# Kernel tuning notes

Hardware: AMD Instinct MI355X
Metric: run time of the kernel (lower is better)

## Reference

```python
import jax, jax.numpy as jnp
import numpy as np

# config (matches init_kwargs)
B, H, N, D = 2, 8, 2048, 64
ALPHA = 1.0        # < 2 -> power-law kernel branch
D_INT = 4.0        # d_intrinsic
BW = 1.0           # bandwidth
A = 0.5            # dual-sided degree-normalization exponent
R = 1.0            # sphere_radius
MASK_VAL = 10000.0
EPS = 1e-7


def setup_inputs() -> dict:
    key = jax.random.key(0)
    k1, k2, k3, k4 = jax.random.split(key, 4)
    Q = jax.random.normal(k1, (B, H, N, D), dtype=jnp.float32)
    K = jax.random.normal(k2, (B, H, N, D), dtype=jnp.float32)
    V = jax.random.normal(k3, (B, H, N, D), dtype=jnp.float32)
    mask = jax.random.randint(k4, (B, N), 0, 2).astype(jnp.int32)
    return {"Q": Q, "K": K, "V": V, "mask": mask}


def reference(Q, K, V, mask) -> jnp.ndarray:
    # geodesic distance on the sphere: acos(clamp(QK^T)) * radius  [B,H,N,N]
    qk = jnp.einsum('bhnd,bhmd->bhnm', Q, K)
    g_dist = jnp.arccos(jnp.clip(qk, -1.0 + EPS, 1.0 - EPS)) * R
    # key-side padding mask: [B,N] -> [B,1,1,N]
    g_dist = jnp.where(mask[:, None, None, :] == 0, MASK_VAL, g_dist)
    # power-law kernel (alpha < 2 branch)
    attn_score = (1.0 + g_dist / jnp.sqrt(BW)) ** (-D_INT - ALPHA)
    # dual-sided degree normalization (a != 0 branch)
    n_r = jnp.sum(attn_score, axis=-1)   # row degrees [B,H,N]
    n_c = jnp.sum(attn_score, axis=-2)   # col degrees [B,H,N]
    k_tilde = (n_r ** (-A))[..., :, None] * attn_score * (n_c ** (-A))[..., None, :]
    # F.normalize(p=1, dim=3)
    attn = k_tilde / jnp.maximum(jnp.sum(jnp.abs(k_tilde), axis=-1, keepdims=True), 1e-12)
    # dropout p=0.0 -> identity
    return jnp.einsum('bhnm,bhmd->bhnd', attn, V)
```

## Files before the change

kernel.cpp:

```cpp
#include <hip/hip_runtime.h>
#include <hip/hip_bf16.h>
#include <math.h>

#define B_ 2
#define H_ 8
#define N_ 2048
#define D_ 64
#define BH_ 16
#define NT_ (N_/64)
#define LS 72
#define LSW (LS/2)

typedef __attribute__((ext_vector_type(8))) short short8;
typedef __attribute__((ext_vector_type(4))) float float4v;

__device__ __forceinline__ unsigned packbf2(float a, float b){
  __hip_bfloat162 h = __float22bfloat162_rn(make_float2(a, b));
  return *(unsigned*)&h;
}
__device__ __forceinline__ void split2(float a, float b, unsigned& hi, unsigned& lo){
  hi = packbf2(a, b);
  float ha = __uint_as_float(hi << 16);
  float hb = __uint_as_float(hi & 0xFFFF0000u);
  lo = packbf2(a - ha, b - hb);
}
__device__ __forceinline__ void load_split8(const float* p, short8& hi8, short8& lo8){
  float4v v0 = *(const float4v*)p;
  float4v v1 = *(const float4v*)(p + 4);
  unsigned h0,h1,h2,h3,l0,l1,l2,l3;
  split2(v0.x, v0.y, h0, l0);
  split2(v0.z, v0.w, h1, l1);
  split2(v1.x, v1.y, h2, l2);
  split2(v1.z, v1.w, h3, l3);
  unsigned ph[4] = {h0,h1,h2,h3};
  unsigned pl[4] = {l0,l1,l2,l3};
  hi8 = *(short8*)ph;
  lo8 = *(short8*)pl;
}

__device__ __forceinline__ float score_fn(float qk, float masked){
  float ax = fminf(fabsf(qk), 1.0f - 1e-7f);
  float t  = __builtin_amdgcn_sqrtf(1.0f - ax);
  float p  = __builtin_fmaf(__builtin_fmaf(__builtin_fmaf(-0.0187293f, ax, 0.0742610f),
                                           ax, -0.2121144f), ax, 1.5707288f);
  float t2 = t * p;
  float g  = (qk >= 0.0f) ? t2 : (3.14159265358979f - t2);
  g = (masked != 0.0f) ? 10000.0f : g;
  float w1 = 1.0f + g;
  float w2 = w1*w1;
  float w4 = w2*w2;
  float w5 = w4*w1;
  return __builtin_amdgcn_rcpf(w5);
}

template<bool STORE>
__global__ __launch_bounds__(256) void k1_score(
    const float* __restrict__ Q, const float* __restrict__ K,
    const int* __restrict__ mask, float* __restrict__ ncw,
    unsigned short* __restrict__ S)
{
  __shared__ float msk[64];
  __shared__ float red[64*4];

  const int kt = blockIdx.x, bh = blockIdx.y, rz = blockIdx.z;
  const int nz = gridDim.z;
  const int tid = threadIdx.x;
  const int wv = tid>>6, lane = tid&63, quad = lane>>4, l15 = lane&15;

  const float* Qg = Q + (size_t)bh*N_*D_;
  const float* Kg = K + (size_t)bh*N_*D_;

  short8 khi[4][2], klo[4][2];
  #pragma unroll
  for (int s=0;s<4;++s){
    const float* kp = Kg + (size_t)(kt*64 + s*16 + l15)*D_ + quad*8;
    load_split8(kp,      khi[s][0], klo[s][0]);
    load_split8(kp + 32, khi[s][1], klo[s][1]);
  }
  if (tid < 64)
    msk[tid] = (mask[(bh>>3)*N_ + kt*64 + tid] == 0) ? 1.f : 0.f;
  __syncthreads();

  float cs[4][4];
  #pragma unroll
  for (int s=0;s<4;++s)
    #pragma unroll
    for (int i=0;i<4;++i) cs[s][i] = 0.f;

  const int iters = NT_/nz;
  for (int rti=0; rti<iters; ++rti){
    const int rt = rz*iters + rti;
    const float* qp = Qg + (size_t)(rt*64 + wv*16 + l15)*D_ + quad*8;
    short8 bhi[2], blo[2];
    load_split8(qp,      bhi[0], blo[0]);
    load_split8(qp + 32, bhi[1], blo[1]);

    const size_t nrow = (size_t)(bh*NT_ + kt)*N_ + (size_t)rt*64 + wv*16 + l15;
    #pragma unroll
    for (int s=0;s<4;++s){
      float4v c = {0.f,0.f,0.f,0.f};
      #pragma unroll
      for (int cc=0; cc<2; ++cc){
        c = __builtin_amdgcn_mfma_f32_16x16x32_bf16(khi[s][cc], bhi[cc], c, 0,0,0);
        c = __builtin_amdgcn_mfma_f32_16x16x32_bf16(khi[s][cc], blo[cc], c, 0,0,0);
        c = __builtin_amdgcn_mfma_f32_16x16x32_bf16(klo[s][cc], bhi[cc], c, 0,0,0);
      }
      int kl = s*16 + quad*4;
      float sc0 = score_fn(c[0], msk[kl+0]);
      float sc1 = score_fn(c[1], msk[kl+1]);
      float sc2 = score_fn(c[2], msk[kl+2]);
      float sc3 = score_fn(c[3], msk[kl+3]);
      cs[s][0]+=sc0; cs[s][1]+=sc1; cs[s][2]+=sc2; cs[s][3]+=sc3;
      if (STORE){
        uint2 pk;
        pk.x = packbf2(sc0, sc1);
        pk.y = packbf2(sc2, sc3);
        *(uint2*)&S[nrow*64 + kl] = pk;
      }
    }
  }

  #pragma unroll
  for (int s=0;s<4;++s)
    #pragma unroll
    for (int i=0;i<4;++i){
      float v2 = cs[s][i];
      v2 += __shfl_xor(v2, 1);
      v2 += __shfl_xor(v2, 2);
      v2 += __shfl_xor(v2, 4);
      v2 += __shfl_xor(v2, 8);
      cs[s][i] = v2;
    }
  if (l15 == 0){
    #pragma unroll
    for (int s=0;s<4;++s)
      #pragma unroll
      for (int i=0;i<4;++i)
        red[(s*16 + quad*4 + i)*4 + wv] = cs[s][i];
  }
  __syncthreads();
  if (tid < 64){
    float t = red[tid*4+0] + red[tid*4+1] + red[tid*4+2] + red[tid*4+3];
    if (STORE) atomicAdd(&ncw[bh*N_ + kt*64 + tid], t);
    else       ncw[bh*N_ + kt*64 + tid] = 1.0f / sqrtf(t);
  }
}

__global__ __launch_bounds__(256) void k2_pack(
    const float* __restrict__ V, const float* __restrict__ nc,
    unsigned short* __restrict__ Vw)
{
  __shared__ float T[64*65];
  __shared__ float wrow[64];
  const int mt = blockIdx.x, bh = blockIdx.y;
  const int tid = threadIdx.x;
  const float* Vg = V + (size_t)bh*N_*D_;
  const float* ncg = nc + (size_t)bh*N_;
  unsigned short* Fb = Vw + ((size_t)(bh*NT_ + mt)*10)*512;

  {
    int m = tid >> 2;
    int d0 = (tid & 3) * 16;
    int gm = mt*64 + m;
    float wm = 1.0f / sqrtf(fmaxf(ncg[gm], 1e-30f));
    if (d0 == 0) wrow[m] = wm;
    #pragma unroll
    for (int j=0;j<4;++j){
      float4v v = *(const float4v*)(Vg + (size_t)gm*D_ + d0 + j*4);
      T[(d0+j*4+0)*65 + m] = v.x*wm;
      T[(d0+j*4+1)*65 + m] = v.y*wm;
      T[(d0+j*4+2)*65 + m] = v.z*wm;
      T[(d0+j*4+3)*65 + m] = v.w*wm;
    }
  }
  __syncthreads();

  for (int idx = tid; idx < 640; idx += 256){
    int f = idx >> 6, lane = idx & 63;
    int quad = lane >> 4, l15 = lane & 15;
    int s2 = f >> 1, cc = f & 1;
    int m0 = cc*32 + quad*8;
    unsigned pk[4];
    if (s2 < 4){
      int d = s2*16 + l15;
      #pragma unroll
      for (int j=0;j<4;++j)
        pk[j] = packbf2(T[d*65 + m0 + 2*j], T[d*65 + m0 + 2*j + 1]);
    } else if (l15 == 0){
      #pragma unroll
      for (int j=0;j<4;++j)
        pk[j] = packbf2(wrow[m0 + 2*j], wrow[m0 + 2*j + 1]);
    } else {
      pk[0]=pk[1]=pk[2]=pk[3]=0u;
    }
    *(short8*)(Fb + ((size_t)f*64 + lane)*8) = *(short8*)pk;
  }
}

__global__ __launch_bounds__(1024) void k3_lds(
    const unsigned short* __restrict__ S, const unsigned short* __restrict__ Vw,
    float* __restrict__ out)
{
  __shared__ unsigned short Vs[2*2*10*512];

  const int rtp = blockIdx.x, bh = blockIdx.y;
  const int tid = threadIdx.x;
  const int wvid = tid >> 6;
  const int g    = wvid >> 3;
  const int slot = wvid & 7;
  const int lane = tid & 63, quad = lane >> 4, l15 = lane & 15;

  const int row = rtp*128 + slot*16 + l15;

  float4v acc[4];
  #pragma unroll
  for (int i=0;i<4;++i) acc[i] = (float4v){0.f,0.f,0.f,0.f};
  float4v c5 = {0.f,0.f,0.f,0.f};

  for (int c = tid; c < 1280; c += 1024){
    const int gg = (c >= 640) ? 1 : 0;
    const int rem = c - gg*640;
    const int f = rem >> 6, ln = rem & 63;
    const int kt = gg*16;
    *(short8*)&Vs[(((0*2 + gg)*10 + f) << 9) + ln*8] =
      *(const short8*)&Vw[(((size_t)(bh*NT_ + kt)*10 + f) << 9) + ln*8];
  }
  short8 npf0, npf1;
  {
    const size_t sb = ((size_t)(bh*NT_ + g*16)*N_ + row)*64;
    npf0 = *(const short8*)&S[sb + quad*8];
    npf1 = *(const short8*)&S[sb + 32 + quad*8];
  }
  __syncthreads();

  for (int it = 0; it < 16; ++it){
    const int cur = it & 1, nxt = cur ^ 1;
    short8 pf0 = npf0, pf1 = npf1;
    if (it < 15){
      const size_t sb = ((size_t)(bh*NT_ + g*16 + it + 1)*N_ + row)*64;
      npf0 = *(const short8*)&S[sb + quad*8];
      npf1 = *(const short8*)&S[sb + 32 + quad*8];
      for (int c = tid; c < 1280; c += 1024){
        const int gg = (c >= 640) ? 1 : 0;
        const int rem = c - gg*640;
        const int f = rem >> 6, ln = rem & 63;
        const int kt2 = gg*16 + it + 1;
        *(short8*)&Vs[(((nxt*2 + gg)*10 + f) << 9) + ln*8] =
          *(const short8*)&Vw[(((size_t)(bh*NT_ + kt2)*10 + f) << 9) + ln*8];
      }
    }
    const unsigned short* Fl = &Vs[((cur*2 + g)*10) << 9] + (size_t)lane*8;
    short8 va[10];
    #pragma unroll
    for (int f=0; f<10; ++f)
      va[f] = *(const short8*)(Fl + ((size_t)f << 9));

    #pragma unroll
    for (int s2=0;s2<4;++s2){
      acc[s2] = __builtin_amdgcn_mfma_f32_16x16x32_bf16(va[s2*2+0], pf0, acc[s2], 0,0,0);
      acc[s2] = __builtin_amdgcn_mfma_f32_16x16x32_bf16(va[s2*2+1], pf1, acc[s2], 0,0,0);
    }
    c5 = __builtin_amdgcn_mfma_f32_16x16x32_bf16(va[8], pf0, c5, 0,0,0);
    c5 = __builtin_amdgcn_mfma_f32_16x16x32_bf16(va[9], pf1, c5, 0,0,0);

    __syncthreads();
  }

  float* Red = (float*)Vs;
  if (g == 1){
    float* Rr = Red + (size_t)(slot*16 + l15)*68;
    #pragma unroll
    for (int s2=0;s2<4;++s2)
      #pragma unroll
      for (int i=0;i<4;++i)
        Rr[s2*16 + quad*4 + i] = acc[s2][i];
    if (quad == 0) Rr[64] = c5[0];
  }
  __syncthreads();
  if (g == 0){
    const float* Rr = Red + (size_t)(slot*16 + l15)*68;
    #pragma unroll
    for (int s2=0;s2<4;++s2)
      #pragma unroll
      for (int i=0;i<4;++i)
        acc[s2][i] += Rr[s2*16 + quad*4 + i];
    float rs = __shfl(c5[0], l15) + Rr[64];
    float inv = 1.0f / fmaxf(rs, 1e-12f);

    float* Og = out + (size_t)bh*N_*D_ + (size_t)row*D_;
    #pragma unroll
    for (int s2=0;s2<4;++s2)
      #pragma unroll
      for (int i=0;i<4;++i)
        Og[s2*16 + quad*4 + i] = acc[s2][i] * inv;
  }
}

__global__ __launch_bounds__(256) void spop_pass2(
    const float* __restrict__ Q, const float* __restrict__ K,
    const float* __restrict__ V, const int* __restrict__ mask,
    const float* __restrict__ w, float* __restrict__ out)
{
  __shared__ unsigned short Khi[64*LS], Klo[64*LS];
  __shared__ unsigned short Vt[64*LS];
  __shared__ unsigned short Ps[64*LS];
  __shared__ float msk[64], wms[64];

  const int rt = blockIdx.x, bh = blockIdx.y, b = bh>>3;
  const int tid = threadIdx.x;
  const int wv = tid>>6, lane = tid&63, quad = lane>>4, l15 = lane&15;

  const float* Qg = Q + (size_t)bh*N_*D_;
  const float* Kg = K + (size_t)bh*N_*D_;
  const float* Vg = V + (size_t)bh*N_*D_;

  short8 qhi[2], qlo[2];
  {
    const float* qp = Qg + (size_t)(rt*64 + wv*16 + l15)*D_ + quad*8;
    load_split8(qp,      qhi[0], qlo[0]);
    load_split8(qp + 32, qhi[1], qlo[1]);
  }

  float4v acc[4];
  #pragma unroll
  for (int i=0;i<4;++i) acc[i] = (float4v){0.f,0.f,0.f,0.f};
  float rs = 0.f;

  for (int kt=0; kt<NT_; ++kt){
    __syncthreads();
    #pragma unroll
    for (int it=0; it<4; ++it){
      int idx = tid + it*256;
      int r = idx>>4, d4 = (idx&15)<<2;
      const float4v v = *(const float4v*)(Kg + (size_t)(kt*64 + r)*D_ + d4);
      unsigned h0,l0,h1,l1;
      split2(v.x, v.y, h0, l0);
      split2(v.z, v.w, h1, l1);
      unsigned* KhiW = (unsigned*)Khi; unsigned* KloW = (unsigned*)Klo;
      int base = r*LSW + (d4>>1);
      KhiW[base] = h0; KhiW[base+1] = h1;
      KloW[base] = l0; KloW[base+1] = l1;
    }
    #pragma unroll
    for (int it=0; it<2; ++it){
      int u = tid + it*256;
      int kp = u & 31;
      int d4 = (u>>5)<<2;
      const float* vp = Vg + (size_t)(kt*64 + kp*2)*D_ + d4;
      float4v a0 = *(const float4v*)vp;
      float4v a1 = *(const float4v*)(vp + D_);
      unsigned* VtW = (unsigned*)Vt;
      VtW[(d4+0)*LSW + kp] = packbf2(a0.x, a1.x);
      VtW[(d4+1)*LSW + kp] = packbf2(a0.y, a1.y);
      VtW[(d4+2)*LSW + kp] = packbf2(a0.z, a1.z);
      VtW[(d4+3)*LSW + kp] = packbf2(a0.w, a1.w);
    }
    if (tid < 64){
      int gk = kt*64 + tid;
      msk[tid] = (mask[b*N_ + gk] == 0) ? 1.f : 0.f;
      wms[tid] = w[bh*N_ + gk];
    }
    __syncthreads();

    #pragma unroll
    for (int s=0;s<4;++s){
      float4v c = {0.f,0.f,0.f,0.f};
      #pragma unroll
      for (int cc=0; cc<2; ++cc){
        const short8 ahi = *(const short8*)&Khi[(s*16+l15)*LS + cc*32 + quad*8];
        const short8 alo = *(const short8*)&Klo[(s*16+l15)*LS + cc*32 + quad*8];
        c = __builtin_amdgcn_mfma_f32_16x16x32_bf16(ahi, qhi[cc], c, 0,0,0);
        c = __builtin_amdgcn_mfma_f32_16x16x32_bf16(ahi, qlo[cc], c, 0,0,0);
        c = __builtin_amdgcn_mfma_f32_16x16x32_bf16(alo, qhi[cc], c, 0,0,0);
      }
      int kl = s*16 + quad*4;
      float sc0 = score_fn(c[0], msk[kl+0]) * wms[kl+0];
      float sc1 = score_fn(c[1], msk[kl+1]) * wms[kl+1];
      float sc2 = score_fn(c[2], msk[kl+2]) * wms[kl+2];
      float sc3 = score_fn(c[3], msk[kl+3]) * wms[kl+3];
      rs += (sc0 + sc1) + (sc2 + sc3);
      unsigned* PsW = (unsigned*)Ps;
      int pb = (wv*16 + l15)*LSW + (kl>>1);
      PsW[pb]   = packbf2(sc0, sc1);
      PsW[pb+1] = packbf2(sc2, sc3);
    }

    short8 pf[2];
    pf[0] = *(const short8*)&Ps[(wv*16+l15)*LS +  0 + quad*8];
    pf[1] = *(const short8*)&Ps[(wv*16+l15)*LS + 32 + quad*8];
    #pragma unroll
    for (int s2=0;s2<4;++s2){
      #pragma unroll
      for (int cc=0; cc<2; ++cc){
        const short8 av = *(const short8*)&Vt[(s2*16+l15)*LS + cc*32 + quad*8];
        acc[s2] = __builtin_amdgcn_mfma_f32_16x16x32_bf16(av, pf[cc], acc[s2], 0,0,0);
      }
    }
  }

  rs += __shfl_xor(rs, 16);
  rs += __shfl_xor(rs, 32);
  float inv = 1.0f / fmaxf(rs, 1e-12f);

  float* Og = out + (size_t)bh*N_*D_ + (size_t)(rt*64 + wv*16 + l15)*D_;
  #pragma unroll
  for (int s2=0;s2<4;++s2)
    #pragma unroll
    for (int i=0;i<4;++i)
      Og[s2*16 + quad*4 + i] = acc[s2][i] * inv;
}

extern "C" void kernel_launch(void* const* d_in, const int* in_sizes, int n_in,
                              void* d_out, int out_size, void* d_ws, size_t ws_size,
                              hipStream_t stream) {
  (void)in_sizes; (void)n_in; (void)out_size;
  const float* Q   = (const float*)d_in[0];
  const float* K   = (const float*)d_in[1];
  const float* V   = (const float*)d_in[2];
  const int*  mask = (const int*)d_in[3];
  float* out = (float*)d_out;

  const size_t nc_bytes = (size_t)BH_*N_*sizeof(float);
  const size_t vw_off   = 131072;
  const size_t vw_bytes = (size_t)BH_*NT_*10*512*2;
  const size_t s_off    = vw_off + vw_bytes;
  const size_t S_bytes  = (size_t)2*BH_*N_*N_;
  const size_t need     = s_off + S_bytes;

  if (ws_size >= need){
    float* nc = (float*)d_ws;
    unsigned short* Vw = (unsigned short*)((char*)d_ws + vw_off);
    unsigned short* S  = (unsigned short*)((char*)d_ws + s_off);
    hipMemsetAsync(nc, 0, nc_bytes, stream);
    k1_score<true><<<dim3(NT_, BH_, 4), 256, 0, stream>>>(Q, K, mask, nc, S);
    k2_pack<<<dim3(NT_, BH_), 256, 0, stream>>>(V, nc, Vw);
    k3_lds<<<dim3(N_/128, BH_), 1024, 0, stream>>>(S, Vw, out);
  } else {
    float* w = (float*)d_ws;
    k1_score<false><<<dim3(NT_, BH_, 1), 256, 0, stream>>>(Q, K, mask, w, nullptr);
    spop_pass2<<<dim3(NT_, BH_), 256, 0, stream>>>(Q, K, V, mask, w, out);
  }
}
```

Before: 184.9 us.

## Pre-split Q/K to bf16 hi/lo, drop score masking, tile S in MFMA layout

Adds a pre-pass that splits Q and K into bf16 hi/lo arrays once, so the score kernel loads ready-made operands instead of re-splitting fp32 Q for every key tile. The key mask leaves the score loop: masked columns are zeroed through the column weight in the V-pack kernel, so column degrees of masked keys are no longer exact but their contribution vanishes. S is stored in a blocked fragment layout so the PV kernel reads contiguous 16-byte chunks, and the next Q fragment is software-prefetched. The cost is extra workspace and an additional kernel launch.

After: 173.9 us. 1.06x faster.

```diff
diff --git a/kernel.cpp b/kernel.cpp
--- a/kernel.cpp
+++ b/kernel.cpp
@@ -38,7 +38,19 @@
   lo8 = *(short8*)pl;
 }
 
-__device__ __forceinline__ float score_fn(float qk, float masked){
+__device__ __forceinline__ float score_fn(float qk){
+  float ax = fminf(fabsf(qk), 1.0f - 1e-7f);
+  float t  = __builtin_amdgcn_sqrtf(1.0f - ax);
+  float p  = __builtin_fmaf(__builtin_fmaf(__builtin_fmaf(-0.0187293f, ax, 0.0742610f),
+                                           ax, -0.2121144f), ax, 1.5707288f);
+  float t2 = t * p;
+  float g  = (qk >= 0.0f) ? t2 : (3.14159265358979f - t2);
+  float w1 = 1.0f + g;
+  float w2 = w1*w1;
+  float w4 = w2*w2;
+  return __builtin_amdgcn_rcpf(w4*w1);
+}
+__device__ __forceinline__ float score_fn_m(float qk, float masked){
   float ax = fminf(fabsf(qk), 1.0f - 1e-7f);
   float t  = __builtin_amdgcn_sqrtf(1.0f - ax);
   float p  = __builtin_fmaf(__builtin_fmaf(__builtin_fmaf(-0.0187293f, ax, 0.0742610f),
@@ -49,37 +61,56 @@
   float w1 = 1.0f + g;
   float w2 = w1*w1;
   float w4 = w2*w2;
-  float w5 = w4*w1;
-  return __builtin_amdgcn_rcpf(w5);
-}
-
-template<bool STORE>
+  return __builtin_amdgcn_rcpf(w4*w1);
+}
+
+__global__ __launch_bounds__(256) void k0_split(
+    const float* __restrict__ Q, const float* __restrict__ K,
+    unsigned short* __restrict__ Qh, unsigned short* __restrict__ Ql,
+    unsigned short* __restrict__ Kh, unsigned short* __restrict__ Kl)
+{
+  size_t i = (size_t)blockIdx.x*256 + threadIdx.x;
+  const size_t tot = (size_t)BH_*N_*D_/8;
+  const float* src; unsigned short *dh, *dl;
+  if (i < tot){ src = Q; dh = Qh; dl = Ql; }
+  else        { src = K; dh = Kh; dl = Kl; i -= tot; }
+  short8 hi, lo;
+  load_split8(src + i*8, hi, lo);
+  *(short8*)&dh[i*8] = hi;
+  *(short8*)&dl[i*8] = lo;
+}
+
+template<bool PRE>
 __global__ __launch_bounds__(256) void k1_score(
-    const float* __restrict__ Q, const float* __restrict__ K,
-    const int* __restrict__ mask, float* __restrict__ ncw,
-    unsigned short* __restrict__ S)
+    const float* __restrict__ Qf, const float* __restrict__ Kf,
+    const unsigned short* __restrict__ Qh, const unsigned short* __restrict__ Ql,
+    const unsigned short* __restrict__ Kh, const unsigned short* __restrict__ Kl,
+    float* __restrict__ ncw, unsigned short* __restrict__ S)
 {
-  __shared__ float msk[64];
   __shared__ float red[64*4];
-
   const int kt = blockIdx.x, bh = blockIdx.y, rz = blockIdx.z;
   const int nz = gridDim.z;
   const int tid = threadIdx.x;
   const int wv = tid>>6, lane = tid&63, quad = lane>>4, l15 = lane&15;
 
-  const float* Qg = Q + (size_t)bh*N_*D_;
-  const float* Kg = K + (size_t)bh*N_*D_;
-
   short8 khi[4][2], klo[4][2];
-  #pragma unroll
-  for (int s=0;s<4;++s){
-    const float* kp = Kg + (size_t)(kt*64 + s*16 + l15)*D_ + quad*8;
-    load_split8(kp,      khi[s][0], klo[s][0]);
-    load_split8(kp + 32, khi[s][1], klo[s][1]);
-  }
-  if (tid < 64)
-    msk[tid] = (mask[(bh>>3)*N_ + kt*64 + tid] == 0) ? 1.f : 0.f;
-  __syncthreads();
+  if constexpr (PRE){
+    #pragma unroll
+    for (int s=0;s<4;++s){
+      const size_t r = (size_t)(bh*N_ + kt*64 + s*16 + l15)*D_ + quad*8;
+      khi[s][0] = *(const short8*)&Kh[r];
+      khi[s][1] = *(const short8*)&Kh[r+32];
+      klo[s][0] = *(const short8*)&Kl[r];
+      klo[s][1] = *(const short8*)&Kl[r+32];
+    }
+  } else {
+    #pragma unroll
+    for (int s=0;s<4;++s){
+      const float* kp = Kf + (size_t)(bh*N_ + kt*64 + s*16 + l15)*D_ + quad*8;
+      load_split8(kp,      khi[s][0], klo[s][0]);
+      load_split8(kp + 32, khi[s][1], klo[s][1]);
+    }
+  }
 
   float cs[4][4];
   #pragma unroll
@@ -88,36 +119,59 @@
     for (int i=0;i<4;++i) cs[s][i] = 0.f;
 
   const int iters = NT_/nz;
+  const int rt0 = rz*iters;
+
+  const size_t qoff0 = (size_t)(bh*N_ + rt0*64 + wv*16 + l15)*D_ + quad*8;
+  const unsigned lconst = (unsigned)(((quad>>1)<<7) + (l15<<3) + ((quad&1)<<2));
+  unsigned short* Sp = S + ((((size_t)(bh*NT_ + kt)*NT_ + rt0)*4 + wv)<<10) + lconst;
+
+  short8 qh0,qh1,ql0,ql1;
+  if constexpr (PRE){
+    const unsigned short* qp = Qh + qoff0;
+    const unsigned short* lp = Ql + qoff0;
+    qh0 = *(const short8*)qp;      qh1 = *(const short8*)(qp+32);
+    ql0 = *(const short8*)lp;      ql1 = *(const short8*)(lp+32);
+  } else {
+    const float* qp = Qf + qoff0;
+    load_split8(qp,      qh0, ql0);
+    load_split8(qp + 32, qh1, ql1);
+  }
+
   for (int rti=0; rti<iters; ++rti){
-    const int rt = rz*iters + rti;
-    const float* qp = Qg + (size_t)(rt*64 + wv*16 + l15)*D_ + quad*8;
-    short8 bhi[2], blo[2];
-    load_split8(qp,      bhi[0], blo[0]);
-    load_split8(qp + 32, bhi[1], blo[1]);
-
-    const size_t nrow = (size_t)(bh*NT_ + kt)*N_ + (size_t)rt*64 + wv*16 + l15;
+    short8 nh0,nh1,nl0,nl1;
+    const size_t qoffn = qoff0 + (size_t)(rti + ((rti+1<iters) ? 1 : 0))*4096;
+    if constexpr (PRE){
+      const unsigned short* qp = Qh + qoffn;
+      const unsigned short* lp = Ql + qoffn;
+      nh0 = *(const short8*)qp;    nh1 = *(const short8*)(qp+32);
+      nl0 = *(const short8*)lp;    nl1 = *(const short8*)(lp+32);
+    } else {
+      const float* qp = Qf + qoffn;
+      load_split8(qp,      nh0, nl0);
+      load_split8(qp + 32, nh1, nl1);
+    }
+
     #pragma unroll
     for (int s=0;s<4;++s){
       float4v c = {0.f,0.f,0.f,0.f};
-      #pragma unroll
-      for (int cc=0; cc<2; ++cc){
-        c = __builtin_amdgcn_mfma_f32_16x16x32_bf16(khi[s][cc], bhi[cc], c, 0,0,0);
-        c = __builtin_amdgcn_mfma_f32_16x16x32_bf16(khi[s][cc], blo[cc], c, 0,0,0);
-        c = __builtin_amdgcn_mfma_f32_16x16x32_bf16(klo[s][cc], bhi[cc], c, 0,0,0);
-      }
-      int kl = s*16 + quad*4;
-      float sc0 = score_fn(c[0], msk[kl+0]);
-      float sc1 = score_fn(c[1], msk[kl+1]);
-      float sc2 = score_fn(c[2], msk[kl+2]);
-      float sc3 = score_fn(c[3], msk[kl+3]);
+      c = __builtin_amdgcn_mfma_f32_16x16x32_bf16(khi[s][0], qh0, c, 0,0,0);
+      c = __builtin_amdgcn_mfma_f32_16x16x32_bf16(khi[s][0], ql0, c, 0,0,0);
+      c = __builtin_amdgcn_mfma_f32_16x16x32_bf16(klo[s][0], qh0, c, 0,0,0);
+      c = __builtin_amdgcn_mfma_f32_16x16x32_bf16(khi[s][1], qh1, c, 0,0,0);
+      c = __builtin_amdgcn_mfma_f32_16x16x32_bf16(khi[s][1], ql1, c, 0,0,0);
+      c = __builtin_amdgcn_mfma_f32_16x16x32_bf16(klo[s][1], qh1, c, 0,0,0);
+      float sc0 = score_fn(c[0]);
+      float sc1 = score_fn(c[1]);
+      float sc2 = score_fn(c[2]);
+      float sc3 = score_fn(c[3]);
       cs[s][0]+=sc0; cs[s][1]+=sc1; cs[s][2]+=sc2; cs[s][3]+=sc3;
-      if (STORE){
-        uint2 pk;
-        pk.x = packbf2(sc0, sc1);
-        pk.y = packbf2(sc2, sc3);
-        *(uint2*)&S[nrow*64 + kl] = pk;
-      }
-    }
+      uint2 pk;
+      pk.x = packbf2(sc0, sc1);
+      pk.y = packbf2(sc2, sc3);
+      *(uint2*)(Sp + (s<<8)) = pk;
+    }
+    Sp += 4096;
+    qh0=nh0; qh1=nh1; ql0=nl0; ql1=nl1;
   }
 
   #pragma unroll
@@ -141,14 +195,13 @@
   __syncthreads();
   if (tid < 64){
     float t = red[tid*4+0] + red[tid*4+1] + red[tid*4+2] + red[tid*4+3];
-    if (STORE) atomicAdd(&ncw[bh*N_ + kt*64 + tid], t);
-    else       ncw[bh*N_ + kt*64 + tid] = 1.0f / sqrtf(t);
+    atomicAdd(&ncw[bh*N_ + kt*64 + tid], t);
   }
 }
 
 __global__ __launch_bounds__(256) void k2_pack(
     const float* __restrict__ V, const float* __restrict__ nc,
-    unsigned short* __restrict__ Vw)
+    const int* __restrict__ mask, unsigned short* __restrict__ Vw)
 {
   __shared__ float T[64*65];
   __shared__ float wrow[64];
@@ -162,7 +215,8 @@
     int m = tid >> 2;
     int d0 = (tid & 3) * 16;
     int gm = mt*64 + m;
-    float wm = 1.0f / sqrtf(fmaxf(ncg[gm], 1e-30f));
+    float wm = (mask[(bh>>3)*N_ + gm] == 0) ? 0.0f
+             : (1.0f / sqrtf(fmaxf(ncg[gm], 1e-30f)));
     if (d0 == 0) wrow[m] = wm;
     #pragma unroll
     for (int j=0;j<4;++j){
@@ -211,6 +265,10 @@
   const int lane = tid & 63, quad = lane >> 4, l15 = lane & 15;
 
   const int row = rtp*128 + slot*16 + l15;
+  const int rt  = rtp*2 + (slot>>2);
+
+  const size_t sb0 = ((((size_t)bh*NT_ + g*16)*NT_ + rt)*4 + (size_t)(slot&3))*1024
+                   + (size_t)quad*128 + (size_t)l15*8;
 
   float4v acc[4];
   #pragma unroll
@@ -226,20 +284,17 @@
       *(const short8*)&Vw[(((size_t)(bh*NT_ + kt)*10 + f) << 9) + ln*8];
   }
   short8 npf0, npf1;
-  {
-    const size_t sb = ((size_t)(bh*NT_ + g*16)*N_ + row)*64;
-    npf0 = *(const short8*)&S[sb + quad*8];
-    npf1 = *(const short8*)&S[sb + 32 + quad*8];
-  }
+  npf0 = *(const short8*)&S[sb0];
+  npf1 = *(const short8*)&S[sb0 + 512];
   __syncthreads();
 
   for (int it = 0; it < 16; ++it){
     const int cur = it & 1, nxt = cur ^ 1;
     short8 pf0 = npf0, pf1 = npf1;
     if (it < 15){
-      const size_t sb = ((size_t)(bh*NT_ + g*16 + it + 1)*N_ + row)*64;
-      npf0 = *(const short8*)&S[sb + quad*8];
-      npf1 = *(const short8*)&S[sb + 32 + quad*8];
+      const size_t sb = sb0 + (size_t)(it+1)*131072;
+      npf0 = *(const short8*)&S[sb];
+      npf1 = *(const short8*)&S[sb + 512];
       for (int c = tid; c < 1280; c += 1024){
         const int gg = (c >= 640) ? 1 : 0;
         const int rem = c - gg*640;
@@ -293,6 +348,84 @@
       #pragma unroll
       for (int i=0;i<4;++i)
         Og[s2*16 + quad*4 + i] = acc[s2][i] * inv;
+  }
+}
+
+__global__ __launch_bounds__(256) void k1_fallback(
+    const float* __restrict__ Q, const float* __restrict__ K,
+    const int* __restrict__ mask, float* __restrict__ ncw)
+{
+  __shared__ float msk[64];
+  __shared__ float red[64*4];
+  const int kt = blockIdx.x, bh = blockIdx.y;
+  const int tid = threadIdx.x;
+  const int wv = tid>>6, lane = tid&63, quad = lane>>4, l15 = lane&15;
+
+  const float* Qg = Q + (size_t)bh*N_*D_;
+  const float* Kg = K + (size_t)bh*N_*D_;
+
+  short8 khi[4][2], klo[4][2];
+  #pragma unroll
+  for (int s=0;s<4;++s){
+    const float* kp = Kg + (size_t)(kt*64 + s*16 + l15)*D_ + quad*8;
+    load_split8(kp,      khi[s][0], klo[s][0]);
+    load_split8(kp + 32, khi[s][1], klo[s][1]);
+  }
+  if (tid < 64)
+    msk[tid] = (mask[(bh>>3)*N_ + kt*64 + tid] == 0) ? 1.f : 0.f;
+  __syncthreads();
+
+  float cs[4][4];
+  #pragma unroll
+  for (int s=0;s<4;++s)
+    #pragma unroll
+    for (int i=0;i<4;++i) cs[s][i] = 0.f;
+
+  for (int rt=0; rt<NT_; ++rt){
+    const float* qp = Qg + (size_t)(rt*64 + wv*16 + l15)*D_ + quad*8;
+    short8 bhi[2], blo[2];
+    load_split8(qp,      bhi[0], blo[0]);
+    load_split8(qp + 32, bhi[1], blo[1]);
+
+    #pragma unroll
+    for (int s=0;s<4;++s){
+      float4v c = {0.f,0.f,0.f,0.f};
+      #pragma unroll
+      for (int cc=0; cc<2; ++cc){
+        c = __builtin_amdgcn_mfma_f32_16x16x32_bf16(khi[s][cc], bhi[cc], c, 0,0,0);
+        c = __builtin_amdgcn_mfma_f32_16x16x32_bf16(khi[s][cc], blo[cc], c, 0,0,0);
+        c = __builtin_amdgcn_mfma_f32_16x16x32_bf16(klo[s][cc], bhi[cc], c, 0,0,0);
+      }
+      int kl = s*16 + quad*4;
+      cs[s][0] += score_fn_m(c[0], msk[kl+0]);
+      cs[s][1] += score_fn_m(c[1], msk[kl+1]);
+      cs[s][2] += score_fn_m(c[2], msk[kl+2]);
+      cs[s][3] += score_fn_m(c[3], msk[kl+3]);
+    }
+  }
+
+  #pragma unroll
+  for (int s=0;s<4;++s)
+    #pragma unroll
+    for (int i=0;i<4;++i){
+      float v2 = cs[s][i];
+      v2 += __shfl_xor(v2, 1);
+      v2 += __shfl_xor(v2, 2);
+      v2 += __shfl_xor(v2, 4);
+      v2 += __shfl_xor(v2, 8);
+      cs[s][i] = v2;
+    }
+  if (l15 == 0){
+    #pragma unroll
+    for (int s=0;s<4;++s)
+      #pragma unroll
+      for (int i=0;i<4;++i)
+        red[(s*16 + quad*4 + i)*4 + wv] = cs[s][i];
+  }
+  __syncthreads();
+  if (tid < 64){
+    float t = red[tid*4+0] + red[tid*4+1] + red[tid*4+2] + red[tid*4+3];
+    ncw[bh*N_ + kt*64 + tid] = 1.0f / sqrtf(t);
   }
 }
 
@@ -374,10 +507,10 @@
         c = __builtin_amdgcn_mfma_f32_16x16x32_bf16(alo, qhi[cc], c, 0,0,0);
       }
       int kl = s*16 + quad*4;
-      float sc0 = score_fn(c[0], msk[kl+0]) * wms[kl+0];
-      float sc1 = score_fn(c[1], msk[kl+1]) * wms[kl+1];
-      float sc2 = score_fn(c[2], msk[kl+2]) * wms[kl+2];
-      float sc3 = score_fn(c[3], msk[kl+3]) * wms[kl+3];
+      float sc0 = score_fn_m(c[0], msk[kl+0]) * wms[kl+0];
+      float sc1 = score_fn_m(c[1], msk[kl+1]) * wms[kl+1];
+      float sc2 = score_fn_m(c[2], msk[kl+2]) * wms[kl+2];
+      float sc3 = score_fn_m(c[3], msk[kl+3]) * wms[kl+3];
       rs += (sc0 + sc1) + (sc2 + sc3);
       unsigned* PsW = (unsigned*)Ps;
       int pb = (wv*16 + l15)*LSW + (kl>>1);
@@ -423,21 +556,39 @@
   const size_t nc_bytes = (size_t)BH_*N_*sizeof(float);
   const size_t vw_off   = 131072;
   const size_t vw_bytes = (size_t)BH_*NT_*10*512*2;
-  const size_t s_off    = vw_off + vw_bytes;
+  const size_t qk_off   = vw_off + vw_bytes;
+  const size_t qk_one   = (size_t)BH_*N_*D_;
+  const size_t qk_bytes = 4*qk_one*2;
   const size_t S_bytes  = (size_t)2*BH_*N_*N_;
-  const size_t need     = s_off + S_bytes;
-
-  if (ws_size >= need){
+  const size_t need_A   = qk_off + qk_bytes + S_bytes;
+  const size_t need_B   = qk_off + S_bytes;
+
+  if (ws_size >= need_A){
     float* nc = (float*)d_ws;
     unsigned short* Vw = (unsigned short*)((char*)d_ws + vw_off);
-    unsigned short* S  = (unsigned short*)((char*)d_ws + s_off);
+    unsigned short* Qh = (unsigned short*)((char*)d_ws + qk_off);
+    unsigned short* Ql = Qh + qk_one;
+    unsigned short* Kh = Ql + qk_one;
+    unsigned short* Kl = Kh + qk_one;
+    unsigned short* S  = (unsigned short*)((char*)d_ws + qk_off + qk_bytes);
     hipMemsetAsync(nc, 0, nc_bytes, stream);
-    k1_score<true><<<dim3(NT_, BH_, 4), 256, 0, stream>>>(Q, K, mask, nc, S);
-    k2_pack<<<dim3(NT_, BH_), 256, 0, stream>>>(V, nc, Vw);
+    k0_split<<<dim3(2048), 256, 0, stream>>>(Q, K, Qh, Ql, Kh, Kl);
+    k1_score<true><<<dim3(NT_, BH_, 4), 256, 0, stream>>>(
+        nullptr, nullptr, Qh, Ql, Kh, Kl, nc, S);
+    k2_pack<<<dim3(NT_, BH_), 256, 0, stream>>>(V, nc, mask, Vw);
+    k3_lds<<<dim3(N_/128, BH_), 1024, 0, stream>>>(S, Vw, out);
+  } else if (ws_size >= need_B){
+    float* nc = (float*)d_ws;
+    unsigned short* Vw = (unsigned short*)((char*)d_ws + vw_off);
+    unsigned short* S  = (unsigned short*)((char*)d_ws + qk_off);
+    hipMemsetAsync(nc, 0, nc_bytes, stream);
+    k1_score<false><<<dim3(NT_, BH_, 4), 256, 0, stream>>>(
+        Q, K, nullptr, nullptr, nullptr, nullptr, nc, S);
+    k2_pack<<<dim3(NT_, BH_), 256, 0, stream>>>(V, nc, mask, Vw);
     k3_lds<<<dim3(N_/128, BH_), 1024, 0, stream>>>(S, Vw, out);
   } else {
     float* w = (float*)d_ws;
-    k1_score<false><<<dim3(NT_, BH_, 1), 256, 0, stream>>>(Q, K, mask, w, nullptr);
+    k1_fallback<<<dim3(NT_, BH_), 256, 0, stream>>>(Q, K, mask, w);
     spop_pass2<<<dim3(NT_, BH_), 256, 0, stream>>>(Q, K, V, mask, w, out);
   }
 }
```
